# Kernel optimization log

Measured on AMD Instinct MI355X. Metric: run time of the kernel, lower is better.

## Reference

```python
import jax, jax.numpy as jnp
import numpy as np

B, S, H, I = 2, 4096, 2048, 8192
K_RATIO = 0.5
K = int(K_RATIO * I)  # 4096 kept activations per token


def setup_inputs() -> dict:
    key = jax.random.key(0)
    kx, kg, ku, kd = jax.random.split(key, 4)
    x = jax.random.normal(kx, (B, S, H), dtype=jnp.float32)
    # nn.Linear(in, out, bias=False) weight has shape [out, in]; y = x @ W.T
    Wg = jax.random.normal(kg, (I, H), dtype=jnp.float32) * (1.0 / np.sqrt(H))
    Wu = jax.random.normal(ku, (I, H), dtype=jnp.float32) * (1.0 / np.sqrt(H))
    Wd = jax.random.normal(kd, (H, I), dtype=jnp.float32) * (1.0 / np.sqrt(I))
    return {"x": x, "Wg": Wg, "Wu": Wu, "Wd": Wd}


def topk_activation(g):
    # Keep top-K entries by magnitude along the last dim, zero the rest.
    ag = jnp.abs(g)
    kth = jax.lax.top_k(ag, K)[0][..., -1:]  # [B,S,1] k-th largest |g|
    return jnp.where(ag >= kth, g, jnp.zeros_like(g))


def reference(x, Wg, Wu, Wd):
    gate = topk_activation(jnp.einsum('bsh,ih->bsi', x, Wg))  # [B,S,I] sparse
    up = jnp.einsum('bsh,ih->bsi', x, Wu)                      # [B,S,I]
    return jnp.einsum('bsi,hi->bsh', gate * up, Wd)            # [B,S,H]
```

## Files before the change

### kernel.cpp

```cpp
#include <hip/hip_runtime.h>

#define T_TOK 8192
#define HDIM  2048
#define IDIM  8192
#define KKEEP 4096
#define TCHK  4096
#define BAND  1.6e-3f
#define MAXB  192

typedef _Float16 f16x8 __attribute__((ext_vector_type(8)));
typedef float    f32x4 __attribute__((ext_vector_type(4)));
typedef ushort   u16x8 __attribute__((ext_vector_type(8)));

#define AS1 __attribute__((address_space(1)))
#define AS3 __attribute__((address_space(3)))
#define BARR asm volatile("s_barrier" ::: "memory")

__device__ __forceinline__ int swzA(int b) {
    return b ^ ((b >> 3) & 0x30) ^ ((b >> 2) & 0x40);
}

union H16 { ushort u; _Float16 h; };


__global__ void cast_f16(const float4* __restrict__ in, ushort4* __restrict__ o, long n4) {
    long stride = (long)gridDim.x * blockDim.x;
    for (long i = (long)blockIdx.x * blockDim.x + threadIdx.x; i < n4; i += stride) {
        float4 v = in[i];
        float vv[4] = {v.x, v.y, v.z, v.w};
        union { _Float16 f[4]; ushort4 u; } H;
        #pragma unroll
        for (int j = 0; j < 4; ++j) H.f[j] = (_Float16)vv[j];
        o[i] = H.u;
    }
}

#define GLOAD(src_, dst_) \
    __builtin_amdgcn_global_load_lds((const AS1 void*)(src_), (AS3 void*)(dst_), 16, 0, 0)


#define STAGE4(pA_, pB_, kt_, buf_) do { \
    char* db_ = Lc + (buf_)*32768 + wave*1024; \
    GLOAD((pA_) + aBase + (kt_) + off0, db_); \
    GLOAD((pA_) + aBase + (kt_) + off1, db_ +  8192); \
    GLOAD((pB_) + bBase + (kt_) + off2, db_ + 16384); \
    GLOAD((pB_) + bBase + (kt_) + off3, db_ + 24576); \
  } while (0)

#define RDFRAG(dstA_, dstB_, tt_) do { \
    const char* bp_ = Lc + ((tt_) & 3) * 32768; \
    _Pragma("unroll") \
    for (int m_ = 0; m_ < 8; ++m_) (dstA_)[m_] = *(const f16x8*)(bp_ + pa + m_ * 1024); \
    _Pragma("unroll") \
    for (int n_ = 0; n_ < 4; ++n_) (dstB_)[n_] = *(const f16x8*)(bp_ + pb + n_ * 1024); \
  } while (0)

#define BODY(t_, curA_, curB_, nxtA_, nxtB_) do { \
    if ((t_) + 2 < NT) asm volatile("s_waitcnt vmcnt(4)" ::: "memory"); \
    else               asm volatile("s_waitcnt vmcnt(0)" ::: "memory"); \
    BARR; \
    if ((t_) + 3 < NT) STAGE4(A0, B0, ((t_) + 3) << 5, ((t_) + 3) & 3); \
    if ((t_) + 1 < NT) RDFRAG(nxtA_, nxtB_, (t_) + 1); \
    __builtin_amdgcn_s_setprio(1); \
    _Pragma("unroll") \
    for (int m_ = 0; m_ < 8; ++m_) \
      _Pragma("unroll") \
      for (int n_ = 0; n_ < 4; ++n_) \
        acc[m_][n_] = __builtin_amdgcn_mfma_f32_16x16x32_f16((curA_)[m_], (curB_)[n_], acc[m_][n_], 0, 0, 0); \
    __builtin_amdgcn_s_setprio(0); \
  } while (0)

template <int MODE>
__global__ __launch_bounds__(512, 2) void gemm4(
    const _Float16* __restrict__ A0, const _Float16* __restrict__ B0,
    int N, int Kp, float* __restrict__ Cf, _Float16* __restrict__ Ch)
{
    __shared__ __align__(128) char Lc[131072];
    const int tid  = threadIdx.x;
    const int lane = tid & 63;
    const int wave = tid >> 6;
    const int wr = wave >> 2, wc = wave & 3;

    const int gx = gridDim.x, gy = gridDim.y;
    const int nwg = gx * gy;
    const int orig = blockIdx.y * gx + blockIdx.x;
    const int q = nwg >> 3, r = nwg & 7, xcd = orig & 7, lid = orig >> 3;
    const int wg = (xcd < r ? xcd * (q + 1) : r * (q + 1) + (xcd - r) * q) + lid;
    const int bm = wg / gy, bn = wg % gy;

    int off0, off1, off2, off3;
    {
        int o[4];
        #pragma unroll
        for (int g = 0; g < 4; ++g) {
            int p = g * 8192 + tid * 16;
            int l = swzA(p);
            int row = (l >> 6) & 255;
            int col = (l & 63) >> 1;
            o[g] = row * Kp + col;
        }
        off0 = o[0]; off1 = o[1]; off2 = o[2]; off3 = o[3];
    }
    const size_t aBase = (size_t)bm * 256 * Kp;
    const size_t bBase = (size_t)bn * 256 * Kp;

    const int l15 = lane & 15, lhi = lane >> 4;
    const int pa = swzA((wr * 128 + l15) * 64 + lhi * 16);
    const int pb = swzA(16384 + (wc * 64 + l15) * 64 + lhi * 16);

    const int NT = Kp >> 5;
    f32x4 acc[8][4] = {};
    f16x8 a0f[8], b0f[4], a1f[8], b1f[4];

    STAGE4(A0, B0, 0,  0);
    STAGE4(A0, B0, 32, 1);
    STAGE4(A0, B0, 64, 2);
    asm volatile("s_waitcnt vmcnt(8)" ::: "memory");
    BARR;
    RDFRAG(a0f, b0f, 0);

    for (int t = 0; t < NT; t += 2) {
        BODY(t,     a0f, b0f, a1f, b1f);
        BODY(t + 1, a1f, b1f, a0f, b0f);
    }

    const int r0 = bm * 256 + wr * 128 + (lane >> 4) * 4;
    const int c0 = bn * 256 + wc * 64 + (lane & 15);
    #pragma unroll
    for (int m = 0; m < 8; ++m) {
        #pragma unroll
        for (int n = 0; n < 4; ++n) {
            #pragma unroll
            for (int rr = 0; rr < 4; ++rr) {
                const size_t idx = (size_t)(r0 + m * 16 + rr) * N + (c0 + n * 16);
                if (MODE == 0) Cf[idx] = acc[m][n][rr];
                else           Ch[idx] = (_Float16)acc[m][n][rr];
            }
        }
    }
}


__global__ __launch_bounds__(256) void topk_sel(
    _Float16* __restrict__ GP, const _Float16* __restrict__ U,
    const float* __restrict__ xf, const float* __restrict__ Wgf)
{
    __shared__ ushort keys[IDIM];
    __shared__ float  xrow[HDIM];
    __shared__ unsigned char bmap[IDIM];
    __shared__ unsigned hist[256], sA_[256], sB_[256];
    __shared__ unsigned selBin, selAbove;
    __shared__ int Acnt, nbv;
    __shared__ int   bidxs[MAXB];
    __shared__ float bval[MAXB];
    __shared__ int   kflag[MAXB];

    const int tid = threadIdx.x;
    const int t = blockIdx.x;
    _Float16* grow = GP + (size_t)t * IDIM;
    const _Float16* urow = U + (size_t)t * IDIM;

    if (tid == 0) { Acnt = 0; nbv = 0; }
    for (int j8 = tid * 8; j8 < IDIM; j8 += 2048) {
        u16x8 v = *(const u16x8*)(grow + j8);
        u16x8 k;
        #pragma unroll
        for (int e = 0; e < 8; ++e) k[e] = (ushort)(v[e] & 0x7FFFu);
        *(u16x8*)(keys + j8) = k;
    }
    for (int j4 = tid; j4 < IDIM / 4; j4 += 256)
        ((unsigned*)bmap)[j4] = 0xFFFFFFFFu;
    for (int j4 = tid * 4; j4 < HDIM; j4 += 1024)
        *(float4*)(xrow + j4) = *(const float4*)(xf + (size_t)t * HDIM + j4);
    __syncthreads();

    unsigned kq = 0;
    int Krem = KKEEP;
    for (int pass = 0; pass < 2; ++pass) {
        const int shift = pass == 0 ? 7 : 0;
        const unsigned msk = pass == 0 ? 255u : 127u;
        hist[tid] = 0;
        __syncthreads();
        for (int j8 = tid * 8; j8 < IDIM; j8 += 2048) {
            u16x8 kv = *(const u16x8*)(keys + j8);
            #pragma unroll
            for (int e = 0; e < 8; ++e) {
                unsigned k = kv[e];
                bool ok = (pass == 0) || ((k >> 7) == (kq >> 7));
                if (ok) atomicAdd(&hist[(k >> shift) & msk], 1u);
            }
        }
        __syncthreads();
        sA_[tid] = hist[tid];
        __syncthreads();
        unsigned *src = sA_, *dst = sB_;
        for (int off = 1; off < 256; off <<= 1) {
            unsigned v = src[tid] + ((tid + off < 256) ? src[tid + off] : 0u);
            dst[tid] = v;
            __syncthreads();
            unsigned* tmp = src; src = dst; dst = tmp;
        }
        unsigned S  = src[tid];
        unsigned Sn = (tid < 255) ? src[tid + 1] : 0u;
        if ((int)S >= Krem && (int)Sn < Krem) { selBin = (unsigned)tid; selAbove = Sn; }
        __syncthreads();
        kq |= selBin << shift;
        Krem -= (int)selAbove;
        __syncthreads();
    }
    H16 cv; cv.u = (ushort)kq;
    const float kthf = (float)cv.h;
    const float hif = kthf + BAND;
    const float lof = kthf - BAND;

    for (int j8 = tid * 8; j8 < IDIM; j8 += 2048) {
        u16x8 kv = *(const u16x8*)(keys + j8);
        #pragma unroll
        for (int e = 0; e < 8; ++e) {
            H16 c; c.u = kv[e];
            float v = (float)c.h;
            if (v > hif) atomicAdd(&Acnt, 1);
            else if (v >= lof) {
                int s = atomicAdd(&nbv, 1);
                if (s < MAXB) { bidxs[s] = j8 + e; bmap[j8 + e] = (unsigned char)s; }
            }
        }
    }
    __syncthreads();

    const int nbc = nbv < MAXB ? nbv : MAXB;
    int R = KKEEP - Acnt;
    R = R < 0 ? 0 : (R > nbc ? nbc : R);

    const int wv = tid >> 6, ln = tid & 63;
    for (int j = wv; j < nbc; j += 4) {
        const float* wrow = Wgf + (size_t)bidxs[j] * HDIM;
        float s = 0.f;
        #pragma unroll
        for (int it = 0; it < HDIM / 256; ++it) {
            const int c = it * 256 + ln * 4;
            float4 w = *(const float4*)(wrow + c);
            float4 xv = *(const float4*)(xrow + c);
            s = fmaf(xv.x, w.x, s);
            s = fmaf(xv.y, w.y, s);
            s = fmaf(xv.z, w.z, s);
            s = fmaf(xv.w, w.w, s);
        }
        #pragma unroll
        for (int o = 32; o; o >>= 1) s += __shfl_xor(s, o);
        if (ln == 0) bval[j] = fabsf(s);
    }
    __syncthreads();

    for (int j = tid; j < nbc; j += 256) {
        int rk = 0;
        float vj = bval[j];
        for (int k = 0; k < nbc; ++k) rk += (bval[k] > vj);
        kflag[j] = (rk < R) ? 1 : 0;
    }
    __syncthreads();

    for (int j8 = tid * 8; j8 < IDIM; j8 += 2048) {
        u16x8 g8 = *(const u16x8*)(grow + j8);
        u16x8 u8 = *(const u16x8*)(urow + j8);
        u16x8 p8;
        #pragma unroll
        for (int e = 0; e < 8; ++e) {
            H16 cg; cg.u = g8[e];
            H16 cu; cu.u = u8[e];
            float g = (float)cg.h;
            float v = fabsf(g);
            bool keep;
            unsigned char s = bmap[j8 + e];
            if (s != 255)      keep = (kflag[s] != 0);
            else if (v > hif)  keep = true;
            else if (v < lof)  keep = false;
            else               keep = (v >= kthf);
            H16 cp; cp.h = keep ? (_Float16)(g * (float)cu.h) : (_Float16)0.f;
            p8[e] = cp.u;
        }
        *(u16x8*)(grow + j8) = p8;
    }
}


extern "C" void kernel_launch(void* const* d_in, const int* in_sizes, int n_in,
                              void* d_out, int out_size, void* d_ws, size_t ws_size,
                              hipStream_t stream) {
    const float* x  = (const float*)d_in[0];
    const float* Wg = (const float*)d_in[1];
    const float* Wu = (const float*)d_in[2];
    const float* Wd = (const float*)d_in[3];

    const size_t NE   = (size_t)T_TOK * HDIM;
    const size_t szH2 = NE * 2;

    char* ws = (char*)d_ws;
    _Float16* xh   = (_Float16*)ws;
    _Float16* Wgh  = (_Float16*)(ws + szH2);
    _Float16* Wu16 = (_Float16*)(ws + 2 * szH2);
    _Float16* Wd16 = (_Float16*)(ws + 3 * szH2);
    _Float16* G    = (_Float16*)(ws + 4 * szH2);
    _Float16* Uc   = (_Float16*)d_out;

    const long n4 = (long)(NE / 4);
    cast_f16<<<1024, 256, 0, stream>>>((const float4*)x,  (ushort4*)xh,   n4);
    cast_f16<<<1024, 256, 0, stream>>>((const float4*)Wg, (ushort4*)Wgh,  n4);
    cast_f16<<<1024, 256, 0, stream>>>((const float4*)Wu, (ushort4*)Wu16, n4);
    cast_f16<<<1024, 256, 0, stream>>>((const float4*)Wd, (ushort4*)Wd16, n4);

    gemm4<1><<<dim3(T_TOK / 256, IDIM / 256), 512, 0, stream>>>(
        xh, Wgh, IDIM, HDIM, nullptr, G);

    for (int c0 = 0; c0 < T_TOK; c0 += TCHK) {
        gemm4<1><<<dim3(TCHK / 256, IDIM / 256), 512, 0, stream>>>(
            xh + (size_t)c0 * HDIM, Wu16, IDIM, HDIM, nullptr, Uc);
        topk_sel<<<TCHK, 256, 0, stream>>>(
            G + (size_t)c0 * IDIM, Uc, x + (size_t)c0 * HDIM, Wg);
    }

    gemm4<0><<<dim3(T_TOK / 256, HDIM / 256), 512, 0, stream>>>(
        G, Wd16, HDIM, IDIM, (float*)d_out, nullptr);
}
```

Measured before the change: 1.243 ms.

## Fuse cast launches, stage fp16 GEMM epilogue through LDS, privatize top-k histogram

Merges the four fp32-to-fp16 cast kernels into one 2D-grid launch. The fp16-output GEMM epilogue now writes accumulators to swizzled LDS, then stores 16-byte vectors row-contiguously, replacing scattered 2-byte global stores. The top-k first-pass histogram uses per-wave private LDS histograms that are then summed, which cuts atomic contention. Costs are an extra barrier and LDS traffic in the epilogue, plus reuse of the staging LDS that must no longer be in use.

Result: slower. 1.287 ms (+3.5%).

```diff
diff --git a/kernel.cpp b/kernel.cpp
--- a/kernel.cpp
+++ b/kernel.cpp
@@ -23,7 +23,17 @@
 union H16 { ushort u; _Float16 h; };
 
 
-__global__ void cast_f16(const float4* __restrict__ in, ushort4* __restrict__ o, long n4) {
+__global__ void cast_all(const float4* __restrict__ x,  const float4* __restrict__ wg,
+                         const float4* __restrict__ wu, const float4* __restrict__ wd,
+                         ushort4* __restrict__ xo,  ushort4* __restrict__ wgo,
+                         ushort4* __restrict__ wuo, ushort4* __restrict__ wdo, long n4) {
+    const float4* in; ushort4* out;
+    switch (blockIdx.y) {
+        case 0:  in = x;  out = xo;  break;
+        case 1:  in = wg; out = wgo; break;
+        case 2:  in = wu; out = wuo; break;
+        default: in = wd; out = wdo; break;
+    }
     long stride = (long)gridDim.x * blockDim.x;
     for (long i = (long)blockIdx.x * blockDim.x + threadIdx.x; i < n4; i += stride) {
         float4 v = in[i];
@@ -31,7 +41,7 @@
         union { _Float16 f[4]; ushort4 u; } H;
         #pragma unroll
         for (int j = 0; j < 4; ++j) H.f[j] = (_Float16)vv[j];
-        o[i] = H.u;
+        out[i] = H.u;
     }
 }
 
@@ -124,18 +134,41 @@
         BODY(t + 1, a1f, b1f, a0f, b0f);
     }
 
-    const int r0 = bm * 256 + wr * 128 + (lane >> 4) * 4;
-    const int c0 = bn * 256 + wc * 64 + (lane & 15);
-    #pragma unroll
-    for (int m = 0; m < 8; ++m) {
-        #pragma unroll
-        for (int n = 0; n < 4; ++n) {
+    if (MODE == 0) {
+        const int r0 = bm * 256 + wr * 128 + (lane >> 4) * 4;
+        const int c0 = bn * 256 + wc * 64 + (lane & 15);
+        #pragma unroll
+        for (int m = 0; m < 8; ++m)
             #pragma unroll
-            for (int rr = 0; rr < 4; ++rr) {
-                const size_t idx = (size_t)(r0 + m * 16 + rr) * N + (c0 + n * 16);
-                if (MODE == 0) Cf[idx] = acc[m][n][rr];
-                else           Ch[idx] = (_Float16)acc[m][n][rr];
+            for (int n = 0; n < 4; ++n)
+                #pragma unroll
+                for (int rr = 0; rr < 4; ++rr)
+                    Cf[(size_t)(r0 + m * 16 + rr) * N + (c0 + n * 16)] = acc[m][n][rr];
+    } else {
+        BARR;
+        char* ep = Lc + wave * 16384;
+        #pragma unroll
+        for (int m = 0; m < 8; ++m) {
+            #pragma unroll
+            for (int n = 0; n < 4; ++n) {
+                #pragma unroll
+                for (int rr = 0; rr < 4; ++rr) {
+                    const int row = m * 16 + (lane >> 4) * 4 + rr;
+                    const int col = n * 16 + (lane & 15);
+                    const int bo = (row * 128 + col * 2) ^ ((row & 7) << 4);
+                    *(_Float16*)(ep + bo) = (_Float16)acc[m][n][rr];
+                }
             }
+        }
+        asm volatile("s_waitcnt lgkmcnt(0)" ::: "memory");
+        const int rg0 = bm * 256 + wr * 128;
+        const int cg0 = bn * 256 + wc * 64 + (lane & 7) * 8;
+        #pragma unroll
+        for (int it = 0; it < 16; ++it) {
+            const int row = it * 8 + (lane >> 3);
+            const int bo = (row * 128 + (lane & 7) * 16) ^ ((row & 7) << 4);
+            f16x8 v = *(const f16x8*)(ep + bo);
+            *(f16x8*)(Ch + (size_t)(rg0 + row) * N + cg0) = v;
         }
     }
 }
@@ -148,6 +181,7 @@
     __shared__ ushort keys[IDIM];
     __shared__ float  xrow[HDIM];
     __shared__ unsigned char bmap[IDIM];
+    __shared__ unsigned hw[4][256];
     __shared__ unsigned hist[256], sA_[256], sB_[256];
     __shared__ unsigned selBin, selAbove;
     __shared__ int Acnt, nbv;
@@ -156,6 +190,7 @@
     __shared__ int   kflag[MAXB];
 
     const int tid = threadIdx.x;
+    const int wv = tid >> 6, ln = tid & 63;
     const int t = blockIdx.x;
     _Float16* grow = GP + (size_t)t * IDIM;
     const _Float16* urow = U + (size_t)t * IDIM;
@@ -172,25 +207,37 @@
         ((unsigned*)bmap)[j4] = 0xFFFFFFFFu;
     for (int j4 = tid * 4; j4 < HDIM; j4 += 1024)
         *(float4*)(xrow + j4) = *(const float4*)(xf + (size_t)t * HDIM + j4);
+    #pragma unroll
+    for (int b = ln; b < 256; b += 64) hw[wv][b] = 0;
+    __syncthreads();
+
+    for (int j8 = tid * 8; j8 < IDIM; j8 += 2048) {
+        u16x8 kv = *(const u16x8*)(keys + j8);
+        #pragma unroll
+        for (int e = 0; e < 8; ++e)
+            atomicAdd(&hw[wv][(kv[e] >> 7) & 255u], 1u);
+    }
+    __syncthreads();
+    hist[tid] = hw[0][tid] + hw[1][tid] + hw[2][tid] + hw[3][tid];
     __syncthreads();
 
     unsigned kq = 0;
     int Krem = KKEEP;
     for (int pass = 0; pass < 2; ++pass) {
         const int shift = pass == 0 ? 7 : 0;
-        const unsigned msk = pass == 0 ? 255u : 127u;
-        hist[tid] = 0;
-        __syncthreads();
-        for (int j8 = tid * 8; j8 < IDIM; j8 += 2048) {
-            u16x8 kv = *(const u16x8*)(keys + j8);
-            #pragma unroll
-            for (int e = 0; e < 8; ++e) {
-                unsigned k = kv[e];
-                bool ok = (pass == 0) || ((k >> 7) == (kq >> 7));
-                if (ok) atomicAdd(&hist[(k >> shift) & msk], 1u);
+        if (pass == 1) {
+            hist[tid] = 0;
+            __syncthreads();
+            for (int j8 = tid * 8; j8 < IDIM; j8 += 2048) {
+                u16x8 kv = *(const u16x8*)(keys + j8);
+                #pragma unroll
+                for (int e = 0; e < 8; ++e) {
+                    unsigned k = kv[e];
+                    if ((k >> 7) == (kq >> 7)) atomicAdd(&hist[k & 127u], 1u);
+                }
             }
-        }
-        __syncthreads();
+            __syncthreads();
+        }
         sA_[tid] = hist[tid];
         __syncthreads();
         unsigned *src = sA_, *dst = sB_;
@@ -232,7 +279,6 @@
     int R = KKEEP - Acnt;
     R = R < 0 ? 0 : (R > nbc ? nbc : R);
 
-    const int wv = tid >> 6, ln = tid & 63;
     for (int j = wv; j < nbc; j += 4) {
         const float* wrow = Wgf + (size_t)bidxs[j] * HDIM;
         float s = 0.f;
@@ -304,10 +350,9 @@
     _Float16* Uc   = (_Float16*)d_out;
 
     const long n4 = (long)(NE / 4);
-    cast_f16<<<1024, 256, 0, stream>>>((const float4*)x,  (ushort4*)xh,   n4);
-    cast_f16<<<1024, 256, 0, stream>>>((const float4*)Wg, (ushort4*)Wgh,  n4);
-    cast_f16<<<1024, 256, 0, stream>>>((const float4*)Wu, (ushort4*)Wu16, n4);
-    cast_f16<<<1024, 256, 0, stream>>>((const float4*)Wd, (ushort4*)Wd16, n4);
+    cast_all<<<dim3(512, 4), 256, 0, stream>>>(
+        (const float4*)x, (const float4*)Wg, (const float4*)Wu, (const float4*)Wd,
+        (ushort4*)xh, (ushort4*)Wgh, (ushort4*)Wu16, (ushort4*)Wd16, n4);
 
     gemm4<1><<<dim3(T_TOK / 256, IDIM / 256), 512, 0, stream>>>(
         xh, Wgh, IDIM, HDIM, nullptr, G);
```
